# Performance work log

Hardware: AMD Instinct MI355X
Metric: run time of the kernel (lower is better)

Reference implementation:

```python
import jax, jax.numpy as jnp
import numpy as np

NUM_HEADS = 12
HEAD_DIM = 64  # hidden 768 / 12


def setup_inputs() -> dict:
    key = jax.random.key(0)
    k1, k2, k3, k4 = jax.random.split(key, 4)
    B, S, H = 8, 1024, 768
    scale = 1.0 / np.sqrt(H)
    hidden_states = jax.random.normal(k1, (B, S, H), dtype=jnp.float32)
    Wq = jax.random.normal(k2, (H, H), dtype=jnp.float32) * scale
    Wk = jax.random.normal(k3, (H, H), dtype=jnp.float32) * scale
    Wv = jax.random.normal(k4, (H, H), dtype=jnp.float32) * scale
    return {"hidden_states": hidden_states, "Wq": Wq, "Wk": Wk, "Wv": Wv}


def reference(hidden_states, Wq, Wk, Wv):
    B, S, H = hidden_states.shape
    nh, hd = NUM_HEADS, HEAD_DIM
    # Linear projections, no bias. torch Linear: x @ W.T with W of shape [out, in];
    # here weights are stored [out, in] == [H, H].
    def proj(W):
        y = jnp.einsum('bsh,oh->bso', hidden_states, W)
        return y.reshape(B, S, nh, hd).transpose(0, 2, 1, 3)  # [B, nh, S, hd]
    q = proj(Wq)
    k = proj(Wk)
    v = proj(Wv)
    scale = 1.0 / np.sqrt(hd).astype(np.float32)
    scores = jnp.einsum('bhqd,bhkd->bhqk', q, k) * scale  # [B, nh, S, S]
    probs = jax.nn.softmax(scores, axis=-1)
    ctx = jnp.einsum('bhqk,bhkd->bhqd', probs, v)  # [B, nh, S, hd]
    ctx = ctx.transpose(0, 2, 1, 3).reshape(B, S, nh * hd)  # [B, S, H]
    return ctx
```

## Files before the change

kernel.cpp:

```cpp
#include <hip/hip_runtime.h>
#include <hip/hip_fp16.h>

typedef _Float16 f16;
typedef _Float16 f16x4 __attribute__((ext_vector_type(4)));
typedef _Float16 f16x8 __attribute__((ext_vector_type(8)));
typedef float f32x4 __attribute__((ext_vector_type(4)));

#define GLB_AS __attribute__((address_space(1)))
#define LDS_AS __attribute__((address_space(3)))

__device__ __forceinline__ void gload_lds16(const f16* g, f16* lds) {
    __builtin_amdgcn_global_load_lds((const GLB_AS uint32_t*)g,
                                     (LDS_AS uint32_t*)lds, 16, 0, 0);
}

__device__ __forceinline__ int swz(int r, int c8) {
    return r * 64 + (((c8) ^ (r & 7)) << 3);
}

__global__ void cvt_all(const float* __restrict__ hs, const float* __restrict__ wq,
                        const float* __restrict__ wk, const float* __restrict__ wv,
                        f16* __restrict__ hs16, f16* __restrict__ w16) {
    int i = blockIdx.x * 256 + threadIdx.x;
    const float4* src;
    f16x8* dst;
    int off;
    if (i < 786432) {
        src = (const float4*)hs; dst = (f16x8*)hs16; off = i;
    } else {
        int j = i - 786432;
        int w = j / 73728;
        off = j - w * 73728;
        src = (const float4*)(w == 0 ? wq : (w == 1 ? wk : wv));
        dst = (f16x8*)(w16 + (size_t)w * 589824);
    }
    float4 a = src[2 * off], c = src[2 * off + 1];
    f16x8 h = {(f16)a.x, (f16)a.y, (f16)a.z, (f16)a.w,
               (f16)c.x, (f16)c.y, (f16)c.z, (f16)c.w};
    dst[off] = h;
}

#define QSCALE 0.18033688011112043f

template <bool SWAP>
__device__ __forceinline__ void gemm_kloop(
        const f16* Abase, const f16* Wbase, f16* As, f16* Bs,
        f32x4 (&acc)[4][4], int wave, int wm, int wn, int quad, int l16,
        int srow, int scol) {
    for (int kt = 0; kt < 12; ++kt) {
        const int k0 = kt * 64;
        __syncthreads();
#pragma unroll
        for (int j = 0; j < 4; ++j) {
            int inst = wave * 4 + j;
            int row = inst * 8 + srow;
            gload_lds16(Abase + (size_t)row * 768 + k0 + scol, &As[inst * 512]);
            gload_lds16(Wbase + (size_t)row * 768 + k0 + scol, &Bs[inst * 512]);
        }
        __syncthreads();
#pragma unroll
        for (int kk = 0; kk < 2; ++kk) {
            f16x8 af[4], bf[4];
#pragma unroll
            for (int mi = 0; mi < 4; ++mi) {
                int r = wm * 64 + mi * 16 + l16;
                af[mi] = *(const f16x8*)&As[swz(r, kk * 4 + quad)];
            }
#pragma unroll
            for (int ni = 0; ni < 4; ++ni) {
                int r = wn * 64 + ni * 16 + l16;
                bf[ni] = *(const f16x8*)&Bs[swz(r, kk * 4 + quad)];
            }
#pragma unroll
            for (int mi = 0; mi < 4; ++mi)
#pragma unroll
                for (int ni = 0; ni < 4; ++ni)
                    acc[mi][ni] = SWAP
                        ? __builtin_amdgcn_mfma_f32_16x16x32_f16(
                              bf[ni], af[mi], acc[mi][ni], 0, 0, 0)
                        : __builtin_amdgcn_mfma_f32_16x16x32_f16(
                              af[mi], bf[ni], acc[mi][ni], 0, 0, 0);
        }
    }
}

__global__ __launch_bounds__(256, 4) void qkv_gemm(
        const f16* __restrict__ A, const f16* __restrict__ W,
        f16* __restrict__ Qh, f16* __restrict__ Kh, f16* __restrict__ Vth) {
    __shared__ f16 As[128 * 64];
    __shared__ f16 Bs[128 * 64];
    const int m0 = blockIdx.x * 128;
    const int n0 = blockIdx.y * 128;
    const int tid = threadIdx.x;
    const int wave = tid >> 6, lane = tid & 63;
    const int wm = wave & 1, wn = wave >> 1;
    const int quad = lane >> 4, l16 = lane & 15;
    const int srow = lane >> 3;
    const int scol = (((lane & 7) ^ srow) << 3);

    f32x4 acc[4][4] = {};
    const f16* Abase = A + (size_t)m0 * 768;
    const f16* Wbase = W + (size_t)n0 * 768;

    const int seg = n0 / 768;
    const int obase = n0 - seg * 768;

    if (seg == 2) {
        gemm_kloop<false>(Abase, Wbase, As, Bs, acc, wave, wm, wn, quad, l16, srow, scol);
#pragma unroll
        for (int mi = 0; mi < 4; ++mi) {
#pragma unroll
            for (int ni = 0; ni < 4; ++ni) {
                int o = obase + wn * 64 + ni * 16 + l16;
                int h = o >> 6, d = o & 63;
                int gm0 = m0 + wm * 64 + mi * 16 + quad * 4;
                int b = gm0 >> 10, s = gm0 & 1023;
                size_t bh = (size_t)(b * 12 + h);
                f16x4 v4 = {(f16)acc[mi][ni][0], (f16)acc[mi][ni][1],
                            (f16)acc[mi][ni][2], (f16)acc[mi][ni][3]};
                *(f16x4*)&Vth[(bh << 16) + ((size_t)d << 10) + s] = v4;
            }
        }
    } else {
        gemm_kloop<true>(Abase, Wbase, As, Bs, acc, wave, wm, wn, quad, l16, srow, scol);
        f16* dst = (seg == 0) ? Qh : Kh;
        const float scale = (seg == 0) ? QSCALE : 1.0f;
#pragma unroll
        for (int mi = 0; mi < 4; ++mi) {
            int gm = m0 + wm * 64 + mi * 16 + l16;
            int b = gm >> 10, s = gm & 1023;
#pragma unroll
            for (int ni = 0; ni < 4; ++ni) {
                int o = obase + wn * 64 + ni * 16 + quad * 4;
                int h = o >> 6, d = o & 63;
                size_t bh = (size_t)(b * 12 + h);
                f16x4 v4 = {(f16)(acc[mi][ni][0] * scale), (f16)(acc[mi][ni][1] * scale),
                            (f16)(acc[mi][ni][2] * scale), (f16)(acc[mi][ni][3] * scale)};
                *(f16x4*)&dst[((bh << 10 | (size_t)s) << 6) + d] = v4;
            }
        }
    }
}

__global__ __launch_bounds__(256, 3) void attn(
        const f16* __restrict__ Qh, const f16* __restrict__ Kh,
        const f16* __restrict__ Vth, float* __restrict__ out) {
    __shared__ __align__(16) char smem[49152];
    f16* Qs  = (f16*)smem;
    f16* Ks  = (f16*)(smem + 16384);
    f16* Vts = (f16*)(smem + 32768);

    const int bh = blockIdx.x;
    const int q0 = blockIdx.y * 128;
    const int b = bh / 12, hh = bh % 12;
    const int tid = threadIdx.x, wave = tid >> 6, lane = tid & 63;
    const int quad = lane >> 4, l16 = lane & 15;
    const int srow = lane >> 3;
    const int scol = (((lane & 7) ^ srow) << 3);

    const f16* qbase = Qh + ((size_t)bh * 1024 + q0) * 64;
    const f16* kbase = Kh + (size_t)bh * 1024 * 64;
    const f16* vtbase = Vth + (size_t)bh * 64 * 1024;

#pragma unroll
    for (int j = 0; j < 4; ++j) {
        int inst = wave * 4 + j;
        int row = inst * 8 + srow;
        gload_lds16(qbase + row * 64 + scol, &Qs[inst * 512]);
    }
#pragma unroll
    for (int j = 0; j < 2; ++j) {
        int inst = wave * 2 + j;
        int row = inst * 8 + srow;
        gload_lds16(kbase + (size_t)row * 64 + scol, &Ks[inst * 512]);
        gload_lds16(vtbase + (size_t)row * 1024 + scol, &Vts[inst * 512]);
    }
    __syncthreads();

    f16x8 qf[2][2];
#pragma unroll
    for (int t = 0; t < 2; ++t)
#pragma unroll
        for (int kk = 0; kk < 2; ++kk)
            qf[t][kk] = *(const f16x8*)&Qs[swz(wave * 32 + t * 16 + l16, kk * 4 + quad)];

    f32x4 o_acc[2][4] = {};
    float rs[2] = {0.f, 0.f};

    for (int kb = 0; kb < 16; ++kb) {
        const int cur = kb & 1;
        if (kb < 15) {
            const int nk0 = (kb + 1) * 64;
#pragma unroll
            for (int j = 0; j < 2; ++j) {
                int inst = wave * 2 + j;
                int row = inst * 8 + srow;
                gload_lds16(kbase + (size_t)(nk0 + row) * 64 + scol,
                            &Ks[(cur ^ 1) * 4096 + inst * 512]);
                gload_lds16(vtbase + (size_t)row * 1024 + nk0 + scol,
                            &Vts[(cur ^ 1) * 4096 + inst * 512]);
            }
        }

        f32x4 st[2][4] = {};
#pragma unroll
        for (int ct = 0; ct < 4; ++ct) {
            f16x8 a0 = *(const f16x8*)&Ks[cur * 4096 + swz(ct * 16 + l16, quad)];
            f16x8 a1 = *(const f16x8*)&Ks[cur * 4096 + swz(ct * 16 + l16, 4 + quad)];
#pragma unroll
            for (int t = 0; t < 2; ++t) {
                st[t][ct] = __builtin_amdgcn_mfma_f32_16x16x32_f16(a0, qf[t][0], st[t][ct], 0, 0, 0);
                st[t][ct] = __builtin_amdgcn_mfma_f32_16x16x32_f16(a1, qf[t][1], st[t][ct], 0, 0, 0);
            }
        }

        f16x4 pv[2][4];
#pragma unroll
        for (int t = 0; t < 2; ++t)
#pragma unroll
            for (int ct = 0; ct < 4; ++ct) {
                float e0 = __builtin_amdgcn_exp2f(st[t][ct][0]);
                float e1 = __builtin_amdgcn_exp2f(st[t][ct][1]);
                float e2 = __builtin_amdgcn_exp2f(st[t][ct][2]);
                float e3 = __builtin_amdgcn_exp2f(st[t][ct][3]);
                rs[t] += (e0 + e1) + (e2 + e3);
                pv[t][ct] = f16x4{(f16)e0, (f16)e1, (f16)e2, (f16)e3};
            }

#pragma unroll
        for (int kc = 0; kc < 4; ++kc) {
            f16x4 vf[4];
#pragma unroll
            for (int ct = 0; ct < 4; ++ct) {
                int r = ct * 16 + l16;
                int c8 = kc * 2 + (quad >> 1);
                vf[ct] = *(const f16x4*)&Vts[cur * 4096 + r * 64 +
                                             ((c8 ^ (r & 7)) << 3) + (quad & 1) * 4];
            }
#pragma unroll
            for (int t = 0; t < 2; ++t)
#pragma unroll
                for (int ct = 0; ct < 4; ++ct)
                    o_acc[t][ct] = __builtin_amdgcn_mfma_f32_16x16x16f16(
                        vf[ct], pv[t][kc], o_acc[t][ct], 0, 0, 0);
        }

        if (kb < 15) __syncthreads();
    }

#pragma unroll
    for (int t = 0; t < 2; ++t) {
        float v = rs[t];
        v += __shfl_xor(v, 16, 64);
        v += __shfl_xor(v, 32, 64);
        float di = 1.0f / v;
        int s = q0 + wave * 32 + t * 16 + l16;
        float* obase_p = &out[((size_t)b * 1024 + s) * 768 + hh * 64 + quad * 4];
#pragma unroll
        for (int ct = 0; ct < 4; ++ct) {
            f32x4 o = o_acc[t][ct];
            o *= di;
            *(f32x4*)&obase_p[ct * 16] = o;
        }
    }
}

extern "C" void kernel_launch(void* const* d_in, const int* in_sizes, int n_in,
                              void* d_out, int out_size, void* d_ws, size_t ws_size,
                              hipStream_t stream) {
    const float* hs = (const float*)d_in[0];
    const float* Wq = (const float*)d_in[1];
    const float* Wk = (const float*)d_in[2];
    const float* Wv = (const float*)d_in[3];
    float* out = (float*)d_out;

    char* ws = (char*)d_ws;
    f16* hs16 = (f16*)ws;
    f16* w16  = (f16*)(ws + 12582912);
    f16* Qh   = (f16*)(ws + 16121856);
    f16* Kh   = (f16*)(ws + 28704768);
    f16* Vth  = (f16*)(ws + 41287680);

    cvt_all<<<3936, 256, 0, stream>>>(hs, Wq, Wk, Wv, hs16, w16);
    qkv_gemm<<<dim3(64, 18), 256, 0, stream>>>(hs16, w16, Qh, Kh, Vth);
    attn<<<dim3(96, 8), 256, 0, stream>>>(Qh, Kh, Vth, out);
    (void)in_sizes; (void)n_in; (void)out_size; (void)ws_size;
}
```

Measured before the change: 156.5 us.

## Double-buffer QKV GEMM LDS tiles with K=32 steps and prefetch

Restructures the QKV projection GEMM k-loop into 24 steps of K=32 with double-buffered LDS tiles, issuing the next tile's global-to-LDS loads before computing on the current one, with a new swizzle for 32-wide rows. This is meant to overlap global memory latency with MFMA work and remove one barrier per iteration. The conversion kernel is also changed to handle one float4 per thread with twice the blocks. The LDS footprint stays the same, but each step does less MFMA work per barrier, and the cvt change adds thread count.

```diff
diff --git a/kernel.cpp b/kernel.cpp
--- a/kernel.cpp
+++ b/kernel.cpp
@@ -16,6 +16,10 @@
 
 __device__ __forceinline__ int swz(int r, int c8) {
     return r * 64 + (((c8) ^ (r & 7)) << 3);
+}
+
+__device__ __forceinline__ int swz32(int r, int c) {
+    return r * 32 + (((c ^ (r & 3)) ^ (((r >> 2) & 1) << 1)) << 3);
 }
 
 __global__ void cvt_all(const float* __restrict__ hs, const float* __restrict__ wq,
@@ -23,20 +27,19 @@
                         f16* __restrict__ hs16, f16* __restrict__ w16) {
     int i = blockIdx.x * 256 + threadIdx.x;
     const float4* src;
-    f16x8* dst;
+    f16x4* dst;
     int off;
-    if (i < 786432) {
-        src = (const float4*)hs; dst = (f16x8*)hs16; off = i;
+    if (i < 1572864) {
+        src = (const float4*)hs; dst = (f16x4*)hs16; off = i;
     } else {
-        int j = i - 786432;
-        int w = j / 73728;
-        off = j - w * 73728;
+        int j = i - 1572864;
+        int w = j / 147456;
+        off = j - w * 147456;
         src = (const float4*)(w == 0 ? wq : (w == 1 ? wk : wv));
-        dst = (f16x8*)(w16 + (size_t)w * 589824);
-    }
-    float4 a = src[2 * off], c = src[2 * off + 1];
-    f16x8 h = {(f16)a.x, (f16)a.y, (f16)a.z, (f16)a.w,
-               (f16)c.x, (f16)c.y, (f16)c.z, (f16)c.w};
+        dst = (f16x4*)(w16 + (size_t)w * 589824);
+    }
+    float4 v = src[off];
+    f16x4 h = {(f16)v.x, (f16)v.y, (f16)v.z, (f16)v.w};
     dst[off] = h;
 }
 
@@ -46,57 +49,73 @@
 __device__ __forceinline__ void gemm_kloop(
         const f16* Abase, const f16* Wbase, f16* As, f16* Bs,
         f32x4 (&acc)[4][4], int wave, int wm, int wn, int quad, int l16,
-        int srow, int scol) {
-    for (int kt = 0; kt < 12; ++kt) {
-        const int k0 = kt * 64;
-        __syncthreads();
-#pragma unroll
-        for (int j = 0; j < 4; ++j) {
-            int inst = wave * 4 + j;
-            int row = inst * 8 + srow;
-            gload_lds16(Abase + (size_t)row * 768 + k0 + scol, &As[inst * 512]);
-            gload_lds16(Wbase + (size_t)row * 768 + k0 + scol, &Bs[inst * 512]);
-        }
-        __syncthreads();
-#pragma unroll
-        for (int kk = 0; kk < 2; ++kk) {
-            f16x8 af[4], bf[4];
-#pragma unroll
-            for (int mi = 0; mi < 4; ++mi) {
-                int r = wm * 64 + mi * 16 + l16;
-                af[mi] = *(const f16x8*)&As[swz(r, kk * 4 + quad)];
-            }
-#pragma unroll
-            for (int ni = 0; ni < 4; ++ni) {
-                int r = wn * 64 + ni * 16 + l16;
-                bf[ni] = *(const f16x8*)&Bs[swz(r, kk * 4 + quad)];
-            }
-#pragma unroll
-            for (int mi = 0; mi < 4; ++mi)
-#pragma unroll
-                for (int ni = 0; ni < 4; ++ni)
-                    acc[mi][ni] = SWAP
-                        ? __builtin_amdgcn_mfma_f32_16x16x32_f16(
-                              bf[ni], af[mi], acc[mi][ni], 0, 0, 0)
-                        : __builtin_amdgcn_mfma_f32_16x16x32_f16(
-                              af[mi], bf[ni], acc[mi][ni], 0, 0, 0);
-        }
+        int lane) {
+    const int r_in = lane >> 2;
+    const int slot = lane & 3;
+
+    int arow[2], acsrc[2];
+#pragma unroll
+    for (int j = 0; j < 2; ++j) {
+        int inst = wave * 2 + j;
+        int r = inst * 16 + r_in;
+        arow[j] = r;
+        acsrc[j] = (slot ^ (r & 3)) ^ (((r >> 2) & 1) << 1);
+    }
+
+#pragma unroll
+    for (int j = 0; j < 2; ++j) {
+        int inst = wave * 2 + j;
+        gload_lds16(Abase + (size_t)arow[j] * 768 + acsrc[j] * 8, &As[inst * 512]);
+        gload_lds16(Wbase + (size_t)arow[j] * 768 + acsrc[j] * 8, &Bs[inst * 512]);
+    }
+    __syncthreads();
+
+    for (int kt = 0; kt < 24; ++kt) {
+        const int cur = kt & 1;
+        if (kt < 23) {
+            const int k0 = (kt + 1) * 32;
+            const int nb = (cur ^ 1) * 4096;
+#pragma unroll
+            for (int j = 0; j < 2; ++j) {
+                int inst = wave * 2 + j;
+                gload_lds16(Abase + (size_t)arow[j] * 768 + k0 + acsrc[j] * 8,
+                            &As[nb + inst * 512]);
+                gload_lds16(Wbase + (size_t)arow[j] * 768 + k0 + acsrc[j] * 8,
+                            &Bs[nb + inst * 512]);
+            }
+        }
+        const int cb = cur * 4096;
+        f16x8 af[4], bf[4];
+#pragma unroll
+        for (int mi = 0; mi < 4; ++mi)
+            af[mi] = *(const f16x8*)&As[cb + swz32(wm * 64 + mi * 16 + l16, quad)];
+#pragma unroll
+        for (int ni = 0; ni < 4; ++ni)
+            bf[ni] = *(const f16x8*)&Bs[cb + swz32(wn * 64 + ni * 16 + l16, quad)];
+#pragma unroll
+        for (int mi = 0; mi < 4; ++mi)
+#pragma unroll
+            for (int ni = 0; ni < 4; ++ni)
+                acc[mi][ni] = SWAP
+                    ? __builtin_amdgcn_mfma_f32_16x16x32_f16(
+                          bf[ni], af[mi], acc[mi][ni], 0, 0, 0)
+                    : __builtin_amdgcn_mfma_f32_16x16x32_f16(
+                          af[mi], bf[ni], acc[mi][ni], 0, 0, 0);
+        if (kt < 23) __syncthreads();
     }
 }
 
 __global__ __launch_bounds__(256, 4) void qkv_gemm(
         const f16* __restrict__ A, const f16* __restrict__ W,
         f16* __restrict__ Qh, f16* __restrict__ Kh, f16* __restrict__ Vth) {
-    __shared__ f16 As[128 * 64];
-    __shared__ f16 Bs[128 * 64];
+    __shared__ f16 As[2 * 128 * 32];
+    __shared__ f16 Bs[2 * 128 * 32];
     const int m0 = blockIdx.x * 128;
     const int n0 = blockIdx.y * 128;
     const int tid = threadIdx.x;
     const int wave = tid >> 6, lane = tid & 63;
     const int wm = wave & 1, wn = wave >> 1;
     const int quad = lane >> 4, l16 = lane & 15;
-    const int srow = lane >> 3;
-    const int scol = (((lane & 7) ^ srow) << 3);
 
     f32x4 acc[4][4] = {};
     const f16* Abase = A + (size_t)m0 * 768;
@@ -106,15 +125,15 @@
     const int obase = n0 - seg * 768;
 
     if (seg == 2) {
-        gemm_kloop<false>(Abase, Wbase, As, Bs, acc, wave, wm, wn, quad, l16, srow, scol);
+        gemm_kloop<false>(Abase, Wbase, As, Bs, acc, wave, wm, wn, quad, l16, lane);
 #pragma unroll
         for (int mi = 0; mi < 4; ++mi) {
+            int gm0 = m0 + wm * 64 + mi * 16 + quad * 4;
+            int b = gm0 >> 10, s = gm0 & 1023;
 #pragma unroll
             for (int ni = 0; ni < 4; ++ni) {
                 int o = obase + wn * 64 + ni * 16 + l16;
                 int h = o >> 6, d = o & 63;
-                int gm0 = m0 + wm * 64 + mi * 16 + quad * 4;
-                int b = gm0 >> 10, s = gm0 & 1023;
                 size_t bh = (size_t)(b * 12 + h);
                 f16x4 v4 = {(f16)acc[mi][ni][0], (f16)acc[mi][ni][1],
                             (f16)acc[mi][ni][2], (f16)acc[mi][ni][3]};
@@ -122,7 +141,7 @@
             }
         }
     } else {
-        gemm_kloop<true>(Abase, Wbase, As, Bs, acc, wave, wm, wn, quad, l16, srow, scol);
+        gemm_kloop<true>(Abase, Wbase, As, Bs, acc, wave, wm, wn, quad, l16, lane);
         f16* dst = (seg == 0) ? Qh : Kh;
         const float scale = (seg == 0) ? QSCALE : 1.0f;
 #pragma unroll
@@ -281,7 +300,7 @@
     f16* Kh   = (f16*)(ws + 28704768);
     f16* Vth  = (f16*)(ws + 41287680);
 
-    cvt_all<<<3936, 256, 0, stream>>>(hs, Wq, Wk, Wv, hs16, w16);
+    cvt_all<<<7872, 256, 0, stream>>>(hs, Wq, Wk, Wv, hs16, w16);
     qkv_gemm<<<dim3(64, 18), 256, 0, stream>>>(hs16, w16, Qh, Kh, Vth);
     attn<<<dim3(96, 8), 256, 0, stream>>>(Qh, Kh, Vth, out);
     (void)in_sizes; (void)n_in; (void)out_size; (void)ws_size;
```

After: 168.0 us. 7.3% more time.
